# Optimization experiments

Hardware: AMD Instinct MI355X
Metric: run time of the kernel (lower is better)

## Reference

```python
import jax, jax.numpy as jnp
import numpy as np

N, F_IN, H, MH = 50000, 128, 128, 256
E = 800000

def _lin_init(key, out_d, in_d, bias=True):
    k1, k2 = jax.random.split(key)
    bound = 1.0 / np.sqrt(in_d)
    W = jax.random.uniform(k1, (out_d, in_d), minval=-bound, maxval=bound, dtype=jnp.float32)
    if bias:
        b = jax.random.uniform(k2, (out_d,), minval=-bound, maxval=bound, dtype=jnp.float32)
        return W, b
    return W, None

def setup_inputs() -> dict:
    key = jax.random.key(0)
    ks = jax.random.split(key, 8)
    x = jax.random.normal(ks[0], (N, F_IN), dtype=jnp.float32)
    edge_index = jax.random.randint(ks[1], (2, E), 0, N, dtype=jnp.int64)
    W1l, b1l = _lin_init(ks[2], H, F_IN, bias=True)   # SAGEConv1 neighbor lin (with bias)
    W1r, _ = _lin_init(ks[3], H, F_IN, bias=False)    # SAGEConv1 root lin (no bias)
    W2l, b2l = _lin_init(ks[4], H, H, bias=True)
    W2r, _ = _lin_init(ks[5], H, H, bias=False)
    Wm1, bm1 = _lin_init(ks[6], MH, 2 * H, bias=True)
    Wm2, bm2 = _lin_init(ks[7], 1, MH, bias=True)
    return {"x": x, "edge_index": edge_index,
            "W1l": W1l, "b1l": b1l, "W1r": W1r,
            "W2l": W2l, "b2l": b2l, "W2r": W2r,
            "Wm1": Wm1, "bm1": bm1, "Wm2": Wm2, "bm2": bm2}

def _sage_conv(x, src, dst, Wl, bl, Wr, num_nodes):
    # mean-aggregate messages x[src] at dst, then lin_l(agg) + lin_r(x)
    agg = jax.ops.segment_sum(x[src], dst, num_segments=num_nodes)
    cnt = jax.ops.segment_sum(jnp.ones((src.shape[0],), x.dtype), dst, num_segments=num_nodes)
    agg = agg / jnp.maximum(cnt, 1.0)[:, None]
    return agg @ Wl.T + bl + x @ Wr.T

def reference(x, edge_index, W1l, b1l, W1r, W2l, b2l, W2r, Wm1, bm1, Wm2, bm2):
    src, dst = edge_index[0], edge_index[1]
    n = x.shape[0]
    h = jax.nn.relu(_sage_conv(x, src, dst, W1l, b1l, W1r, n))
    # dropout is identity in eval mode
    h = jax.nn.relu(_sage_conv(h, src, dst, W2l, b2l, W2r, n))
    ef = jnp.concatenate([h[src], h[dst]], axis=-1)  # [E, 2H]
    out = jax.nn.relu(ef @ Wm1.T + bm1) @ Wm2.T + bm2
    return out.reshape(-1)
```

## Files before the change

### kernel.cpp

```cpp
#include <hip/hip_runtime.h>
#include <hip/hip_bf16.h>

#define NN 50000
#define F 128
#define EE 800000
#define MHD 256
#define CAP 44

typedef __attribute__((ext_vector_type(8))) short bf16x8;
typedef __attribute__((ext_vector_type(4))) float f32x4;

__device__ __forceinline__ float b2f(unsigned short u) {
    union { unsigned int i; float f; } v; v.i = ((unsigned)u) << 16; return v.f;
}
__device__ __forceinline__ unsigned short f2b(float f) {
    unsigned int x = __float_as_uint(f);
    unsigned int r = x + 0x7fffu + ((x >> 16) & 1u);
    return (unsigned short)(r >> 16);
}

__global__ __launch_bounds__(256) void zero_kernel(
    int* __restrict__ cnt, const float* __restrict__ Wm2, float* __restrict__ w2p) {
    int bid = blockIdx.x;
    if (bid < 49) {
        int idx = (bid * 256 + threadIdx.x) * 4;
        if (idx < NN) *(int4*)(cnt + idx) = (int4){0, 0, 0, 0};
    } else {
        int t = threadIdx.x;
        w2p[t] = Wm2[(t & 15) * 16 + (t >> 4)];
    }
}

__global__ __launch_bounds__(256) void prep_kernel(
    const int* __restrict__ ei, int* __restrict__ cnt,
    unsigned short* __restrict__ slots,
    const float* __restrict__ x,
    const float* __restrict__ W1l, const float* __restrict__ W1r,
    const float* __restrict__ W2l, const float* __restrict__ W2r,
    const float* __restrict__ Wm1,
    unsigned short* __restrict__ xb, unsigned short* __restrict__ wb) {
    int bid = blockIdx.x;
    if (bid < 3125) {
        __shared__ int isI64;
        if (threadIdx.x == 0) {
            int z = 0;
            for (int i = 1; i < 128; i += 2) z |= ei[i];
            isI64 = (z == 0) ? 1 : 0;
        }
        __syncthreads();
        int e = bid * 256 + threadIdx.x;
        if (e >= EE) return;
        int s, d;
        if (isI64) {
            const long long* e64 = (const long long*)ei;
            s = (int)e64[e];
            d = (int)e64[EE + e];
        } else {
            s = ei[e];
            d = ei[EE + e];
        }
        int pos = atomicAdd(&cnt[d], 1);
        if (pos < CAP) {
            unsigned short* sp = slots + (size_t)d * (CAP * 3) + pos * 3;
            sp[0] = (unsigned short)s;
            sp[1] = (unsigned short)(e & 0xffff);
            sp[2] = (unsigned short)((unsigned)e >> 16);
        }
    } else if (bid < 9375) {
        int i = ((bid - 3125) * 256 + threadIdx.x) * 4;
        float4 v = *(const float4*)(x + i);
        ushort4 o; o.x = f2b(v.x); o.y = f2b(v.y); o.z = f2b(v.z); o.w = f2b(v.w);
        *(ushort4*)(xb + i) = o;
    } else {
        int i = ((bid - 9375) * 256 + threadIdx.x) * 4;
        unsigned short o[4];
        if (i < 32768) {
            const float* p = (i < 16384) ? (W1l + i) : (W1r + (i - 16384));
            float4 v = *(const float4*)p;
            o[0] = f2b(v.x); o[1] = f2b(v.y); o[2] = f2b(v.z); o[3] = f2b(v.w);
        } else if (i < 65536) {
            int local = i - 32768;
            const float* M = (local < 16384) ? W2l : W2r;
            int lm = local & 16383;
            int n = lm >> 7, kp = lm & 127;
#pragma unroll
            for (int t = 0; t < 4; t++) {
                int k = ((kp + t) & 7) * 16 + ((kp + t) >> 3);
                o[t] = f2b(M[n * 128 + k]);
            }
        } else {
            int local = i - 65536;
            int n = local >> 8, k2 = local & 255;
            int half = k2 >> 7, kp = k2 & 127;
#pragma unroll
            for (int t = 0; t < 4; t++) {
                int k = half * 128 + ((kp + t) & 7) * 16 + ((kp + t) >> 3);
                o[t] = f2b(Wm1[n * 256 + k]);
            }
        }
        *(ushort4*)(wb + i) = *(ushort4*)o;
    }
}

__global__ __launch_bounds__(256) void sage_layer_kernel(
    const unsigned short* __restrict__ xin,
    const unsigned short* __restrict__ slots, const int* __restrict__ cnt,
    const unsigned short* __restrict__ W1, const unsigned short* __restrict__ W2,
    const float* __restrict__ bias,
    unsigned short* __restrict__ out) {
    __shared__ unsigned short lds[4][16][136];
    int wave = threadIdx.x >> 6, lane = threadIdx.x & 63;
    int m0 = (blockIdx.x * 4 + wave) * 16;

    int g = lane >> 4, l16 = lane & 15, col8 = l16 * 8;
    for (int batch = 0; batch < 4; batch++) {
        int node = m0 + batch * 4 + g;
        int n = 0, ctrue = 0;
        const unsigned short* sp = slots;
        if (node < NN) {
            ctrue = cnt[node];
            n = (ctrue < CAP) ? ctrue : CAP;
            sp = slots + (size_t)node * (CAP * 3);
        }
        float a[8] = {0,0,0,0,0,0,0,0};
        float b[8] = {0,0,0,0,0,0,0,0};
        int j = 0;
        for (; j + 7 < n; j += 8) {
            int s0 = sp[(j + 0) * 3], s1 = sp[(j + 1) * 3];
            int s2 = sp[(j + 2) * 3], s3 = sp[(j + 3) * 3];
            int s4 = sp[(j + 4) * 3], s5 = sp[(j + 5) * 3];
            int s6 = sp[(j + 6) * 3], s7 = sp[(j + 7) * 3];
            bf16x8 v0 = *(const bf16x8*)(xin + (size_t)s0 * F + col8);
            bf16x8 v1 = *(const bf16x8*)(xin + (size_t)s1 * F + col8);
            bf16x8 v2 = *(const bf16x8*)(xin + (size_t)s2 * F + col8);
            bf16x8 v3 = *(const bf16x8*)(xin + (size_t)s3 * F + col8);
            bf16x8 v4 = *(const bf16x8*)(xin + (size_t)s4 * F + col8);
            bf16x8 v5 = *(const bf16x8*)(xin + (size_t)s5 * F + col8);
            bf16x8 v6 = *(const bf16x8*)(xin + (size_t)s6 * F + col8);
            bf16x8 v7 = *(const bf16x8*)(xin + (size_t)s7 * F + col8);
            for (int i = 0; i < 8; i++)
                a[i] += (b2f((unsigned short)v0[i]) + b2f((unsigned short)v1[i]))
                      + (b2f((unsigned short)v2[i]) + b2f((unsigned short)v3[i]));
            for (int i = 0; i < 8; i++)
                b[i] += (b2f((unsigned short)v4[i]) + b2f((unsigned short)v5[i]))
                      + (b2f((unsigned short)v6[i]) + b2f((unsigned short)v7[i]));
        }
        for (; j + 3 < n; j += 4) {
            int s0 = sp[(j + 0) * 3], s1 = sp[(j + 1) * 3];
            int s2 = sp[(j + 2) * 3], s3 = sp[(j + 3) * 3];
            bf16x8 v0 = *(const bf16x8*)(xin + (size_t)s0 * F + col8);
            bf16x8 v1 = *(const bf16x8*)(xin + (size_t)s1 * F + col8);
            bf16x8 v2 = *(const bf16x8*)(xin + (size_t)s2 * F + col8);
            bf16x8 v3 = *(const bf16x8*)(xin + (size_t)s3 * F + col8);
            for (int i = 0; i < 8; i++)
                a[i] += (b2f((unsigned short)v0[i]) + b2f((unsigned short)v1[i]))
                      + (b2f((unsigned short)v2[i]) + b2f((unsigned short)v3[i]));
        }
        for (; j < n; j++) {
            int s0 = sp[j * 3];
            bf16x8 v0 = *(const bf16x8*)(xin + (size_t)s0 * F + col8);
            for (int i = 0; i < 8; i++) a[i] += b2f((unsigned short)v0[i]);
        }
        float inv = 1.0f / fmaxf((float)ctrue, 1.0f);
        unsigned short o[8];
        for (int i = 0; i < 8; i++) o[i] = f2b((a[i] + b[i]) * inv);
        *(bf16x8*)&lds[wave][batch * 4 + g][col8] = *(bf16x8*)o;
    }
    __syncthreads();

    int c = lane & 15, q = lane >> 4;
    f32x4 acc[8];
    for (int nt = 0; nt < 8; nt++) {
        float b = bias[nt * 16 + c];
        acc[nt] = (f32x4){b, b, b, b};
    }
    int mrow = m0 + c; if (mrow > NN - 1) mrow = NN - 1;
    for (int op = 0; op < 2; op++) {
        const unsigned short* W = op ? W2 : W1;
        for (int kb = 0; kb < 4; kb++) {
            bf16x8 a;
            if (op == 0) a = *(const bf16x8*)&lds[wave][c][kb * 32 + q * 8];
            else         a = *(const bf16x8*)(xin + (size_t)mrow * F + kb * 32 + q * 8);
            for (int nt = 0; nt < 8; nt++) {
                bf16x8 b = *(const bf16x8*)(W + (size_t)(nt * 16 + c) * F + kb * 32 + q * 8);
                acc[nt] = __builtin_amdgcn_mfma_f32_16x16x32_bf16(a, b, acc[nt], 0, 0, 0);
            }
        }
    }
#pragma unroll
    for (int r = 0; r < 4; r++) {
        int node = m0 + q * 4 + r;
        if (node < NN) {
            unsigned short o[8];
#pragma unroll
            for (int nt = 0; nt < 8; nt++) o[nt] = f2b(fmaxf(acc[nt][r], 0.0f));
            *(bf16x8*)(out + (size_t)node * F + c * 8) = *(bf16x8*)o;
        }
    }
}

__global__ __launch_bounds__(256) void pq_gemm_kernel(
    const unsigned short* __restrict__ h,
    const unsigned short* __restrict__ wmb,
    const float* __restrict__ bm1,
    unsigned short* __restrict__ PQ) {
    int wave = threadIdx.x >> 6, lane = threadIdx.x & 63;
    int c = lane & 15, q = lane >> 4;
    int half = wave >> 1, ntBase = (wave & 1) * 8;
    int m0 = blockIdx.x * 64;
    int mr0 = m0 + c;      if (mr0 > NN - 1) mr0 = NN - 1;
    int mr1 = m0 + 16 + c; if (mr1 > NN - 1) mr1 = NN - 1;
    int mr2 = m0 + 32 + c; if (mr2 > NN - 1) mr2 = NN - 1;
    int mr3 = m0 + 48 + c; if (mr3 > NN - 1) mr3 = NN - 1;
    f32x4 acc0[8], acc1[8], acc2[8], acc3[8];
#pragma unroll
    for (int nt = 0; nt < 8; nt++) {
        float b = half ? bm1[(ntBase + nt) * 16 + c] : 0.0f;
        acc0[nt] = (f32x4){b, b, b, b};
        acc1[nt] = (f32x4){b, b, b, b};
        acc2[nt] = (f32x4){b, b, b, b};
        acc3[nt] = (f32x4){b, b, b, b};
    }
#pragma unroll
    for (int kb = 0; kb < 4; kb++) {
        bf16x8 a0 = *(const bf16x8*)(h + (size_t)mr0 * F + kb * 32 + q * 8);
        bf16x8 a1 = *(const bf16x8*)(h + (size_t)mr1 * F + kb * 32 + q * 8);
        bf16x8 a2 = *(const bf16x8*)(h + (size_t)mr2 * F + kb * 32 + q * 8);
        bf16x8 a3 = *(const bf16x8*)(h + (size_t)mr3 * F + kb * 32 + q * 8);
#pragma unroll
        for (int nt = 0; nt < 8; nt++) {
            bf16x8 b = *(const bf16x8*)(wmb + (size_t)((ntBase + nt) * 16 + c) * 256 + half * 128 + kb * 32 + q * 8);
            acc0[nt] = __builtin_amdgcn_mfma_f32_16x16x32_bf16(a0, b, acc0[nt], 0, 0, 0);
            acc1[nt] = __builtin_amdgcn_mfma_f32_16x16x32_bf16(a1, b, acc1[nt], 0, 0, 0);
            acc2[nt] = __builtin_amdgcn_mfma_f32_16x16x32_bf16(a2, b, acc2[nt], 0, 0, 0);
            acc3[nt] = __builtin_amdgcn_mfma_f32_16x16x32_bf16(a3, b, acc3[nt], 0, 0, 0);
        }
    }
#pragma unroll
    for (int r = 0; r < 4; r++) {
        int n0 = m0 + q * 4 + r;
        int n1 = m0 + 16 + q * 4 + r;
        int n2 = m0 + 32 + q * 4 + r;
        int n3 = m0 + 48 + q * 4 + r;
        unsigned short o[8];
        if (n0 < NN) {
#pragma unroll
            for (int nt = 0; nt < 8; nt++) o[nt] = f2b(acc0[nt][r]);
            *(bf16x8*)(PQ + (size_t)n0 * 512 + half * 256 + c * 16 + ntBase) = *(bf16x8*)o;
        }
        if (n1 < NN) {
#pragma unroll
            for (int nt = 0; nt < 8; nt++) o[nt] = f2b(acc1[nt][r]);
            *(bf16x8*)(PQ + (size_t)n1 * 512 + half * 256 + c * 16 + ntBase) = *(bf16x8*)o;
        }
        if (n2 < NN) {
#pragma unroll
            for (int nt = 0; nt < 8; nt++) o[nt] = f2b(acc2[nt][r]);
            *(bf16x8*)(PQ + (size_t)n2 * 512 + half * 256 + c * 16 + ntBase) = *(bf16x8*)o;
        }
        if (n3 < NN) {
#pragma unroll
            for (int nt = 0; nt < 8; nt++) o[nt] = f2b(acc3[nt][r]);
            *(bf16x8*)(PQ + (size_t)n3 * 512 + half * 256 + c * 16 + ntBase) = *(bf16x8*)o;
        }
    }
}

__global__ __launch_bounds__(256) void edge_dot_kernel(
    const unsigned short* __restrict__ PQ,
    const unsigned short* __restrict__ slots, const int* __restrict__ cnt,
    const float* __restrict__ w2p, const float* __restrict__ bm2,
    float* __restrict__ out) {
    int wave = threadIdx.x >> 6, lane = threadIdx.x & 63;
    int node = blockIdx.x * 4 + wave;
    if (node >= NN) return;
    int g = lane >> 4, l16 = lane & 15;
    int col = l16 * 16;
    float w2f[16], qf[16];
    *(float4*)(w2f + 0)  = *(const float4*)(w2p + col + 0);
    *(float4*)(w2f + 4)  = *(const float4*)(w2p + col + 4);
    *(float4*)(w2f + 8)  = *(const float4*)(w2p + col + 8);
    *(float4*)(w2f + 12) = *(const float4*)(w2p + col + 12);
    {
        bf16x8 q0 = *(const bf16x8*)(PQ + (size_t)node * 512 + 256 + col);
        bf16x8 q1 = *(const bf16x8*)(PQ + (size_t)node * 512 + 256 + col + 8);
#pragma unroll
        for (int i = 0; i < 8; i++) { qf[i] = b2f((unsigned short)q0[i]); qf[8 + i] = b2f((unsigned short)q1[i]); }
    }
    float b2 = bm2[0];
    int ctrue = cnt[node];
    int n = (ctrue < CAP) ? ctrue : CAP;
    const unsigned short* sp = slots + (size_t)node * (CAP * 3);
    int j = g;
    for (; j + 4 < n; j += 8) {
        int s0 = sp[j * 3],       s1 = sp[(j + 4) * 3];
        int eid0 = sp[j * 3 + 1] | ((int)sp[j * 3 + 2] << 16);
        int eid1 = sp[(j + 4) * 3 + 1] | ((int)sp[(j + 4) * 3 + 2] << 16);
        uint4 a0 = *(const uint4*)(PQ + (size_t)s0 * 512 + col);
        uint4 a1 = *(const uint4*)(PQ + (size_t)s0 * 512 + col + 8);
        uint4 c0 = *(const uint4*)(PQ + (size_t)s1 * 512 + col);
        uint4 c1 = *(const uint4*)(PQ + (size_t)s1 * 512 + col + 8);
        float t0 = 0.f, t1 = 0.f;
        unsigned int w0[8] = {a0.x, a0.y, a0.z, a0.w, a1.x, a1.y, a1.z, a1.w};
        unsigned int w1[8] = {c0.x, c0.y, c0.z, c0.w, c1.x, c1.y, c1.z, c1.w};
#pragma unroll
        for (int i = 0; i < 8; i++) {
            float lo0 = __uint_as_float(w0[i] << 16);
            float hi0 = __uint_as_float(w0[i] & 0xffff0000u);
            float lo1 = __uint_as_float(w1[i] << 16);
            float hi1 = __uint_as_float(w1[i] & 0xffff0000u);
            t0 += fmaxf(lo0 + qf[2 * i], 0.f) * w2f[2 * i]
                + fmaxf(hi0 + qf[2 * i + 1], 0.f) * w2f[2 * i + 1];
            t1 += fmaxf(lo1 + qf[2 * i], 0.f) * w2f[2 * i]
                + fmaxf(hi1 + qf[2 * i + 1], 0.f) * w2f[2 * i + 1];
        }
        t0 += __shfl_xor(t0, 1);  t1 += __shfl_xor(t1, 1);
        t0 += __shfl_xor(t0, 2);  t1 += __shfl_xor(t1, 2);
        t0 += __shfl_xor(t0, 4);  t1 += __shfl_xor(t1, 4);
        t0 += __shfl_xor(t0, 8);  t1 += __shfl_xor(t1, 8);
        if (l16 == 0) { out[eid0] = t0 + b2; out[eid1] = t1 + b2; }
    }
    for (; j < n; j += 4) {
        int s0 = sp[j * 3];
        int eid0 = sp[j * 3 + 1] | ((int)sp[j * 3 + 2] << 16);
        uint4 a0 = *(const uint4*)(PQ + (size_t)s0 * 512 + col);
        uint4 a1 = *(const uint4*)(PQ + (size_t)s0 * 512 + col + 8);
        unsigned int w0[8] = {a0.x, a0.y, a0.z, a0.w, a1.x, a1.y, a1.z, a1.w};
        float t = 0.f;
#pragma unroll
        for (int i = 0; i < 8; i++) {
            float lo = __uint_as_float(w0[i] << 16);
            float hi = __uint_as_float(w0[i] & 0xffff0000u);
            t += fmaxf(lo + qf[2 * i], 0.f) * w2f[2 * i]
               + fmaxf(hi + qf[2 * i + 1], 0.f) * w2f[2 * i + 1];
        }
        t += __shfl_xor(t, 1);
        t += __shfl_xor(t, 2);
        t += __shfl_xor(t, 4);
        t += __shfl_xor(t, 8);
        if (l16 == 0) out[eid0] = t + b2;
    }
}

extern "C" void kernel_launch(void* const* d_in, const int* in_sizes, int n_in,
                              void* d_out, int out_size, void* d_ws, size_t ws_size,
                              hipStream_t stream) {
    const float* x   = (const float*)d_in[0];
    const int*   ei  = (const int*)d_in[1];
    const float* W1l = (const float*)d_in[2];
    const float* b1l = (const float*)d_in[3];
    const float* W1r = (const float*)d_in[4];
    const float* W2l = (const float*)d_in[5];
    const float* b2l = (const float*)d_in[6];
    const float* W2r = (const float*)d_in[7];
    const float* Wm1 = (const float*)d_in[8];
    const float* bm1 = (const float*)d_in[9];
    const float* Wm2 = (const float*)d_in[10];
    const float* bm2 = (const float*)d_in[11];

    char* ws = (char*)d_ws;
    unsigned short* PQ    = (unsigned short*)(ws);
    unsigned short* xb    = (unsigned short*)(ws);
    unsigned short* h1    = (unsigned short*)(ws + 12800000);
    unsigned short* wb    = (unsigned short*)(ws + 51200000);
    float*          w2p   = (float*)(ws + 51462144);
    int*            cnt   = (int*)(ws + 51463168);
    unsigned short* slots = (unsigned short*)(ws + 51663168);
    unsigned short* h2    = (unsigned short*)(ws + 64863168);
    float*          outp  = (float*)d_out;

    const unsigned short* w1l_b  = wb;
    const unsigned short* w1r_b  = wb + 16384;
    const unsigned short* w2l_p  = wb + 32768;
    const unsigned short* w2r_p  = wb + 49152;
    const unsigned short* wm1_p  = wb + 65536;

    zero_kernel<<<50, 256, 0, stream>>>(cnt, Wm2, w2p);
    prep_kernel<<<9503, 256, 0, stream>>>(ei, cnt, slots, x, W1l, W1r, W2l, W2r, Wm1, xb, wb);

    sage_layer_kernel<<<782, 256, 0, stream>>>(xb, slots, cnt, w1l_b, w1r_b, b1l, h1);
    sage_layer_kernel<<<782, 256, 0, stream>>>(h1, slots, cnt, w2l_p, w2r_p, b2l, h2);
    pq_gemm_kernel<<<782, 256, 0, stream>>>(h2, wm1_p, bm1, PQ);
    edge_dot_kernel<<<12500, 256, 0, stream>>>(PQ, slots, cnt, w2p, bm2, outp);
}
```

Baseline: 362.5 us.

## Build CSR slots via two-pass bucketed binning instead of global atomics

Edge-to-destination slot construction now runs in two passes. The first bins edges into 49 coarse cells of 1024 nodes, using shared-memory histograms and one global atomic per cell per block, spread over 8 sub-buckets. A new build kernel then scans each cell's buckets, assembles the per-node slot lists in LDS and writes them out with coalesced stores. This removes 800K scattered global atomics and 6-byte scattered writes, but adds an extra kernel and redundant scanning: each block reads the whole cell, so every cell is read about 8 times. Slot order within a node also changes, and fixed sub-bucket capacities could drop edges if a bucket overflows.

```diff
diff --git a/kernel.cpp b/kernel.cpp
--- a/kernel.cpp
+++ b/kernel.cpp
@@ -6,6 +6,10 @@
 #define EE 800000
 #define MHD 256
 #define CAP 44
+#define NCELL 49
+#define SUBS 8
+#define SUBCAP 2304
+#define CELLCAP (SUBS * SUBCAP)
 
 typedef __attribute__((ext_vector_type(8))) short bf16x8;
 typedef __attribute__((ext_vector_type(4))) float f32x4;
@@ -20,11 +24,11 @@
 }
 
 __global__ __launch_bounds__(256) void zero_kernel(
-    int* __restrict__ cnt, const float* __restrict__ Wm2, float* __restrict__ w2p) {
+    int* __restrict__ gcnt, const float* __restrict__ Wm2, float* __restrict__ w2p) {
     int bid = blockIdx.x;
-    if (bid < 49) {
+    if (bid < 7) {
         int idx = (bid * 256 + threadIdx.x) * 4;
-        if (idx < NN) *(int4*)(cnt + idx) = (int4){0, 0, 0, 0};
+        if (idx < NCELL * SUBS * 16) *(int4*)(gcnt + idx) = (int4){0, 0, 0, 0};
     } else {
         int t = threadIdx.x;
         w2p[t] = Wm2[(t & 15) * 16 + (t >> 4)];
@@ -32,8 +36,8 @@
 }
 
 __global__ __launch_bounds__(256) void prep_kernel(
-    const int* __restrict__ ei, int* __restrict__ cnt,
-    unsigned short* __restrict__ slots,
+    const int* __restrict__ ei, int* __restrict__ gcnt,
+    int2* __restrict__ bkt,
     const float* __restrict__ x,
     const float* __restrict__ W1l, const float* __restrict__ W1r,
     const float* __restrict__ W2l, const float* __restrict__ W2r,
@@ -42,29 +46,43 @@
     int bid = blockIdx.x;
     if (bid < 3125) {
         __shared__ int isI64;
-        if (threadIdx.x == 0) {
+        __shared__ int hist[NCELL];
+        __shared__ int base[NCELL];
+        __shared__ int lpos[NCELL];
+        int t = threadIdx.x;
+        if (t < NCELL) { hist[t] = 0; lpos[t] = 0; }
+        if (t == 0) {
             int z = 0;
             for (int i = 1; i < 128; i += 2) z |= ei[i];
             isI64 = (z == 0) ? 1 : 0;
         }
         __syncthreads();
-        int e = bid * 256 + threadIdx.x;
-        if (e >= EE) return;
-        int s, d;
-        if (isI64) {
-            const long long* e64 = (const long long*)ei;
-            s = (int)e64[e];
-            d = (int)e64[EE + e];
-        } else {
-            s = ei[e];
-            d = ei[EE + e];
-        }
-        int pos = atomicAdd(&cnt[d], 1);
-        if (pos < CAP) {
-            unsigned short* sp = slots + (size_t)d * (CAP * 3) + pos * 3;
-            sp[0] = (unsigned short)s;
-            sp[1] = (unsigned short)(e & 0xffff);
-            sp[2] = (unsigned short)((unsigned)e >> 16);
+        int e = bid * 256 + t;
+        int valid = (e < EE);
+        int s = 0, d = 0, c = 0;
+        if (valid) {
+            if (isI64) {
+                const long long* e64 = (const long long*)ei;
+                s = (int)e64[e];
+                d = (int)e64[EE + e];
+            } else {
+                s = ei[e];
+                d = ei[EE + e];
+            }
+            c = d >> 10;
+            atomicAdd(&hist[c], 1);
+        }
+        __syncthreads();
+        if (t < NCELL && hist[t] > 0)
+            base[t] = atomicAdd(&gcnt[(t * SUBS + (bid & 7)) * 16], hist[t]);
+        __syncthreads();
+        if (valid) {
+            int lp = atomicAdd(&lpos[c], 1);
+            int idx = base[c] + lp;
+            if (idx < SUBCAP) {
+                bkt[(size_t)c * CELLCAP + (bid & 7) * SUBCAP + idx] =
+                    make_int2((int)((unsigned)s | ((unsigned)d << 16)), e);
+            }
         }
     } else if (bid < 9375) {
         int i = ((bid - 3125) * 256 + threadIdx.x) * 4;
@@ -99,6 +117,48 @@
             }
         }
         *(ushort4*)(wb + i) = *(ushort4*)o;
+    }
+}
+
+__global__ __launch_bounds__(256) void build_kernel(
+    const int* __restrict__ gcnt, const int2* __restrict__ bkt,
+    unsigned short* __restrict__ slots, int* __restrict__ cnt2) {
+    __shared__ unsigned short stg[128][132];
+    __shared__ int lcnt[128];
+    int b = blockIdx.x, t = threadIdx.x;
+    int node0 = b * 128;
+    int c = node0 >> 10;
+    if (t < 128) lcnt[t] = 0;
+    __syncthreads();
+#pragma unroll
+    for (int k = 0; k < SUBS; k++) {
+        int n = gcnt[(c * SUBS + k) * 16];
+        if (n > SUBCAP) n = SUBCAP;
+        const int2* seg = bkt + (size_t)c * CELLCAP + k * SUBCAP;
+        for (int i = t; i < n; i += 256) {
+            int2 en = seg[i];
+            unsigned v = (unsigned)en.x;
+            int dl = (int)(v >> 16) - node0;
+            if (dl >= 0 && dl < 128) {
+                int pos = atomicAdd(&lcnt[dl], 1);
+                if (pos < CAP) {
+                    stg[dl][pos * 3 + 0] = (unsigned short)(v & 0xffffu);
+                    stg[dl][pos * 3 + 1] = (unsigned short)(en.y & 0xffff);
+                    stg[dl][pos * 3 + 2] = (unsigned short)((unsigned)en.y >> 16);
+                }
+            }
+        }
+    }
+    __syncthreads();
+    for (int v = t; v < 128 * 33; v += 256) {
+        int row = v / 33, off = (v % 33) * 4;
+        int node = node0 + row;
+        if (node < NN)
+            *(ushort4*)(slots + (size_t)node * 132 + off) = *(ushort4*)&stg[row][off];
+    }
+    if (t < 128) {
+        int node = node0 + t;
+        if (node < NN) cnt2[node] = lcnt[t];
     }
 }
 
@@ -362,11 +422,13 @@
     unsigned short* PQ    = (unsigned short*)(ws);
     unsigned short* xb    = (unsigned short*)(ws);
     unsigned short* h1    = (unsigned short*)(ws + 12800000);
+    int2*           bkt   = (int2*)(ws + 25600000);
     unsigned short* wb    = (unsigned short*)(ws + 51200000);
     float*          w2p   = (float*)(ws + 51462144);
-    int*            cnt   = (int*)(ws + 51463168);
-    unsigned short* slots = (unsigned short*)(ws + 51663168);
-    unsigned short* h2    = (unsigned short*)(ws + 64863168);
+    int*            cnt2  = (int*)(ws + 51463168);
+    int*            gcnt  = (int*)(ws + 51663168);
+    unsigned short* slots = (unsigned short*)(ws + 51688256);
+    unsigned short* h2    = (unsigned short*)(ws + 64888256);
     float*          outp  = (float*)d_out;
 
     const unsigned short* w1l_b  = wb;
@@ -375,11 +437,12 @@
     const unsigned short* w2r_p  = wb + 49152;
     const unsigned short* wm1_p  = wb + 65536;
 
-    zero_kernel<<<50, 256, 0, stream>>>(cnt, Wm2, w2p);
-    prep_kernel<<<9503, 256, 0, stream>>>(ei, cnt, slots, x, W1l, W1r, W2l, W2r, Wm1, xb, wb);
-
-    sage_layer_kernel<<<782, 256, 0, stream>>>(xb, slots, cnt, w1l_b, w1r_b, b1l, h1);
-    sage_layer_kernel<<<782, 256, 0, stream>>>(h1, slots, cnt, w2l_p, w2r_p, b2l, h2);
+    zero_kernel<<<8, 256, 0, stream>>>(gcnt, Wm2, w2p);
+    prep_kernel<<<9503, 256, 0, stream>>>(ei, gcnt, bkt, x, W1l, W1r, W2l, W2r, Wm1, xb, wb);
+    build_kernel<<<391, 256, 0, stream>>>(gcnt, bkt, slots, cnt2);
+
+    sage_layer_kernel<<<782, 256, 0, stream>>>(xb, slots, cnt2, w1l_b, w1r_b, b1l, h1);
+    sage_layer_kernel<<<782, 256, 0, stream>>>(h1, slots, cnt2, w2l_p, w2r_p, b2l, h2);
     pq_gemm_kernel<<<782, 256, 0, stream>>>(h2, wm1_p, bm1, PQ);
-    edge_dot_kernel<<<12500, 256, 0, stream>>>(PQ, slots, cnt, w2p, bm2, outp);
-}
+    edge_dot_kernel<<<12500, 256, 0, stream>>>(PQ, slots, cnt2, w2p, bm2, outp);
+}
```

Result: no change. 360.8 us (-0.5%).
